# Kernel optimization log

Hardware: AMD Instinct MI355X
Metric: run time of the kernel (lower is better)

Reference implementation:

```python
import jax, jax.numpy as jnp
import numpy as np

K = 9          # kernel_size
PAD = K // 2   # 'same' padding, stride 1
SIGMA = 1.0
EPS = 1e-5     # BatchNorm eps

def _windows(a):
    # a: (B, C, L) -> (B, C, K, L); zero-padded sliding windows (== F.unfold semantics)
    L = a.shape[-1]
    ap = jnp.pad(a, ((0, 0), (0, 0), (PAD, PAD)))
    return jnp.stack([ap[:, :, k:k + L] for k in range(K)], axis=2)

def setup_inputs() -> dict:
    key = jax.random.key(0)
    ks = jax.random.split(key, 4)
    B, Cin, Cout, L = 8, 256, 256, 16384
    x = jax.random.normal(ks[0], (B, Cin, L), jnp.float32)
    coords = jax.random.uniform(ks[1], (B, 3, L), jnp.float32)
    conv_w = jax.random.normal(ks[2], (Cout, Cin, K), jnp.float32) * np.float32(1.0 / np.sqrt(Cin * K))
    conv_b = jnp.zeros((Cout,), jnp.float32)
    gamma = jnp.ones((Cout,), jnp.float32)
    beta = jnp.zeros((Cout,), jnp.float32)
    return {"x": x, "coords": coords, "conv_w": conv_w, "conv_b": conv_b, "gamma": gamma, "beta": beta}

def reference(x, coords, conv_w, conv_b, gamma, beta):
    # --- WeightedConv1D: Gaussian coordinate weights on each unfolded window element ---
    cw = _windows(coords)                                      # (B, 3, K, L)
    d2 = jnp.sum((cw - coords[:, :, None, :]) ** 2, axis=1)    # (B, K, L) squared dist to window center
    w = jnp.exp(-d2 / (2.0 * SIGMA ** 2))                      # (B, K, L) Gaussian weights
    xw = _windows(x) * w[:, None, :, :]                        # (B, Cin, K, L) weighted windows
    y = jnp.einsum('bckl,ock->bol', xw, conv_w) + conv_b[None, :, None]  # (B, Cout, L)
    # --- BatchNorm1d (training-mode batch statistics, biased variance) + ReLU ---
    mu = jnp.mean(y, axis=(0, 2), keepdims=True)
    var = jnp.var(y, axis=(0, 2), keepdims=True)
    yhat = (y - mu) * jax.lax.rsqrt(var + EPS)
    out = jax.nn.relu(yhat * gamma[None, :, None] + beta[None, :, None])
    # Dropout with drop=0.0 is the identity.
    return out
```

## Files before the change

### kernel.cpp

```cpp
#include <hip/hip_runtime.h>
#include <hip/hip_bf16.h>


typedef float        f32x4  __attribute__((ext_vector_type(4)));
typedef float        f32x2  __attribute__((ext_vector_type(2)));
typedef short        bf16x8 __attribute__((ext_vector_type(8)));
typedef unsigned int u32x4  __attribute__((ext_vector_type(4)));

#define LLEN 16384

__device__ __forceinline__ unsigned short bf16bits(float a) {
  return __builtin_bit_cast(unsigned short, __float2bfloat16(a));
}
__device__ __forceinline__ unsigned cvt_pk_bf16(float lo, float hi) {
  unsigned r;
  asm("v_cvt_pk_bf16_f32 %0, %1, %2" : "=v"(r) : "v"(lo), "v"(hi));
  return r;
}

__global__ void k_prep(const float* __restrict__ cw,
                       unsigned short* __restrict__ Aperm,
                       float* __restrict__ sums) {
  const int idx = blockIdx.x * 256 + threadIdx.x;
  if (idx < 512) sums[idx] = 0.0f;
  const int o   = idx / 2304;
  const int rem = idx - o * 2304;
  const int c   = rem / 9;
  const int kk  = rem - c * 9;
  Aperm[((size_t)kk * 256 + o) * 256 + c] = bf16bits(cw[idx]);
}

__global__ void k_w(const float* __restrict__ coords, float* __restrict__ wbuf) {
  const int gidx = blockIdx.x * 256 + threadIdx.x;
  const int b = gidx >> 14, l = gidx & (LLEN - 1);
  const float* cb = coords + (size_t)b * 3 * LLEN;
  const float c0 = cb[l], c1 = cb[LLEN + l], c2v = cb[2 * LLEN + l];
#pragma unroll
  for (int kk = 0; kk < 9; ++kk) {
    const int lc = l + kk - 4;
    float a0 = 0.f, a1 = 0.f, a2 = 0.f;
    if (lc >= 0 && lc < LLEN) { a0 = cb[lc]; a1 = cb[LLEN + lc]; a2 = cb[2 * LLEN + lc]; }
    const float d0 = a0 - c0, d1 = a1 - c1, d2 = a2 - c2v;
    wbuf[(((size_t)(b * 9 + kk)) << 14) + l] = __expf(-0.5f * (d0 * d0 + d1 * d1 + d2 * d2));
  }
}

__global__ __launch_bounds__(512, 2) void k_gemm(
    const float* __restrict__ x, const float* __restrict__ wbuf,
    const unsigned short* __restrict__ Aperm, const float* __restrict__ convb,
    float* __restrict__ y, float* __restrict__ sums) {
  __shared__ __align__(16) unsigned short Ash[2][256 * 64];
  __shared__ __align__(16) unsigned short Xsh[2][264 * 72];

  const int tid  = threadIdx.x;
  const int lane = tid & 63, wv = tid >> 6;
  const int wm = wv >> 2, wn = wv & 3;
  const int hi = lane >> 4, lo16 = lane & 15;
  const int b  = blockIdx.x >> 6, lt = blockIdx.x & 63;
  const int l0 = lt << 8;
  const int nbase = wn * 64 + lo16;
  const int c = tid >> 3, rg = tid & 7;

  f32x4 acc[8][4];
#pragma unroll
  for (int i = 0; i < 8; ++i)
#pragma unroll
    for (int j = 0; j < 4; ++j) acc[i][j] = f32x4{0.f, 0.f, 0.f, 0.f};

  auto loadA = [&](int kk, int cc, u32x4 (&dst)[4]) {
#pragma unroll
    for (int p = 0; p < 4; ++p) {
      const int row = p * 64 + (tid >> 3);
      dst[p] = *reinterpret_cast<const u32x4*>(
          Aperm + ((size_t)kk * 256 + row) * 256 + cc * 64 + ((tid & 7) << 3));
    }
  };
  auto writeA = [&](int ab, const u32x4 (&src)[4]) {
#pragma unroll
    for (int p = 0; p < 4; ++p) {
      const int row  = p * 64 + (tid >> 3);
      const unsigned byte = (unsigned)(row * 128 + (((tid & 7) ^ (row & 7)) << 4));
      *reinterpret_cast<u32x4*>(reinterpret_cast<char*>(&Ash[ab][0]) + byte) = src[p];
    }
  };
  auto loadPiece = [&](int ncc, int i) -> f32x4 {
    const float* xrow = x + ((size_t)(b * 256 + ncc * 64 + c)) * LLEN;
    const int grp = rg + 8 * i;
    const int lx = l0 - 4 + grp * 4;
    f32x4 v = {0.f, 0.f, 0.f, 0.f};
    if (grp < 66 && lx >= 0 && lx <= LLEN - 4)
      v = *reinterpret_cast<const f32x4*>(xrow + lx);
    return v;
  };
  auto writePiece = [&](int xb, int i, const f32x4& v) {
    const int grp = rg + 8 * i;
    if (grp < 66) {
      unsigned short* base = &Xsh[xb][0] + (grp * 4) * 72 + c;
      base[0]   = bf16bits(v[0]);
      base[72]  = bf16bits(v[1]);
      base[144] = bf16bits(v[2]);
      base[216] = bf16bits(v[3]);
    }
  };

  {
    u32x4 a0[4];
    loadA(0, 0, a0);
    writeA(0, a0);
#pragma unroll
    for (int i = 0; i < 9; ++i) writePiece(0, i, loadPiece(0, i));
  }
  float wl[4];
#pragma unroll
  for (int nt = 0; nt < 4; ++nt)
    wl[nt] = wbuf[((size_t)(b * 9) << 14) + l0 + nbase + nt * 16];
  __syncthreads();

  int ab = 0;
  f32x4 xhold = {0.f, 0.f, 0.f, 0.f};

#pragma unroll 1
  for (int cc = 0; cc < 4; ++cc) {
    const int xb = cc & 1;
#pragma unroll 1
    for (int kk = 0; kk < 9; ++kk) {
      const int nkk = (kk == 8) ? 0 : kk + 1;
      const int ncc = (kk == 8) ? cc + 1 : cc;
      const bool has_next = (ncc < 4);

      u32x4 areg[4];
      if (has_next) loadA(nkk, ncc, areg);
      float wln[4] = {0.f, 0.f, 0.f, 0.f};
      if (has_next) {
#pragma unroll
        for (int nt = 0; nt < 4; ++nt)
          wln[nt] = wbuf[((size_t)(b * 9 + nkk) << 14) + l0 + nbase + nt * 16];
      }
      f32x4 xnew = {0.f, 0.f, 0.f, 0.f};
      if (cc < 3) xnew = loadPiece(cc + 1, kk);

      const char* AshB = reinterpret_cast<const char*>(&Ash[ab][0]);
      const char* XshB = reinterpret_cast<const char*>(&Xsh[xb][0]);
#pragma unroll
      for (int kb = 0; kb < 2; ++kb) {
        bf16x8 bfr[4];
#pragma unroll
        for (int nt = 0; nt < 4; ++nt) {
          const int r = nbase + nt * 16 + kk;
          const u32x4 xv = *reinterpret_cast<const u32x4*>(XshB + r * 144 + kb * 64 + hi * 16);
          const float wv2 = wl[nt];
          u32x4 o4;
#pragma unroll
          for (int q = 0; q < 4; ++q) {
            f32x2 f = {__builtin_bit_cast(float, xv[q] << 16),
                       __builtin_bit_cast(float, xv[q] & 0xffff0000u)};
            f *= wv2;
            o4[q] = cvt_pk_bf16(f[0], f[1]);
          }
          bfr[nt] = __builtin_bit_cast(bf16x8, o4);
        }
#pragma unroll
        for (int mt = 0; mt < 8; ++mt) {
          const int orow = wm * 128 + mt * 16 + lo16;
          const unsigned aoff = (unsigned)(orow * 128 + (((kb * 4 + hi) ^ (orow & 7)) << 4));
          const bf16x8 af = *reinterpret_cast<const bf16x8*>(AshB + aoff);
#pragma unroll
          for (int nt = 0; nt < 4; ++nt)
            acc[mt][nt] = __builtin_amdgcn_mfma_f32_16x16x32_bf16(af, bfr[nt],
                                                                  acc[mt][nt], 0, 0, 0);
        }
      }

      if (cc < 3 && kk >= 1) writePiece(xb ^ 1, kk - 1, xhold);
      if (cc < 3 && kk == 8) writePiece(xb ^ 1, 8, xnew);
      if (has_next) writeA(ab ^ 1, areg);

      __syncthreads();
      ab ^= 1;
      xhold = xnew;
#pragma unroll
      for (int nt = 0; nt < 4; ++nt) wl[nt] = wln[nt];
    }
  }

  float* red = reinterpret_cast<float*>(&Ash[0][0]);
  red[tid] = 0.0f;
  __syncthreads();
#pragma unroll
  for (int mt = 0; mt < 8; ++mt) {
#pragma unroll
    for (int v = 0; v < 4; ++v) {
      const int o = wm * 128 + mt * 16 + hi * 4 + v;
      const float cb = convb[o];
      float s = 0.f, s2 = 0.f;
#pragma unroll
      for (int nt = 0; nt < 4; ++nt) {
        const int l = l0 + nbase + nt * 16;
        const float yv = acc[mt][nt][v] + cb;
        y[(((size_t)b * 256 + o) << 14) + l] = yv;
        s += yv; s2 += yv * yv;
      }
#pragma unroll
      for (int d = 1; d < 16; d <<= 1) { s += __shfl_xor(s, d); s2 += __shfl_xor(s2, d); }
      if (lo16 == 0) { atomicAdd(&red[o], s); atomicAdd(&red[o + 256], s2); }
    }
  }
  __syncthreads();
  atomicAdd(&sums[tid], red[tid]);
}

__global__ void k_norm(float* __restrict__ y, const float* __restrict__ sums,
                       const float* __restrict__ gamma, const float* __restrict__ beta) {
  const size_t i0 = ((size_t)blockIdx.x * 256 + threadIdx.x) * 8;
  const int o = (int)((i0 >> 14) & 255);
  const float n = 131072.f;
  const float mu = sums[o] / n;
  float var = sums[256 + o] / n - mu * mu;
  var = fmaxf(var, 0.f);
  const float sc = rsqrtf(var + 1e-5f) * gamma[o];
  const float bb = beta[o] - mu * sc;
  f32x4 v0 = *reinterpret_cast<const f32x4*>(y + i0);
  f32x4 v1 = *reinterpret_cast<const f32x4*>(y + i0 + 4);
#pragma unroll
  for (int i = 0; i < 4; ++i) {
    v0[i] = fmaxf(v0[i] * sc + bb, 0.f);
    v1[i] = fmaxf(v1[i] * sc + bb, 0.f);
  }
  *reinterpret_cast<f32x4*>(y + i0) = v0;
  *reinterpret_cast<f32x4*>(y + i0 + 4) = v1;
}

extern "C" void kernel_launch(void* const* d_in, const int* in_sizes, int n_in,
                              void* d_out, int out_size, void* d_ws, size_t ws_size,
                              hipStream_t stream) {
  const float* x      = (const float*)d_in[0];
  const float* coords = (const float*)d_in[1];
  const float* conv_w = (const float*)d_in[2];
  const float* conv_b = (const float*)d_in[3];
  const float* gamma  = (const float*)d_in[4];
  const float* beta   = (const float*)d_in[5];
  float* out = (float*)d_out;

  float* sums = (float*)d_ws;
  float* wbuf = (float*)((char*)d_ws + 4096);
  unsigned short* Aperm =
      (unsigned short*)((char*)d_ws + 4096 + (size_t)8 * 9 * LLEN * 4);

  k_prep<<<2304, 256, 0, stream>>>(conv_w, Aperm, sums);
  k_w<<<512, 256, 0, stream>>>(coords, wbuf);
  k_gemm<<<512, 512, 0, stream>>>(x, wbuf, Aperm, conv_b, out, sums);
  k_norm<<<16384, 256, 0, stream>>>(out, sums, gamma, beta);
}
```

Baseline: 247.0 us.

## Add pre-transposed bf16 x and direct global-to-LDS DMA GEMM path

Adds a kernel that converts x to bf16 and transposes it into an L-major, swizzled layout, plus a pre-swizzled weight copy, so the GEMM can fill LDS with global_load_lds DMA instead of register-staged loads. The GEMM switches from 16x16x32 to 32x32x16 MFMA tiles and uses a zero buffer for boundary padding. The new path runs only when the workspace is large enough; otherwise the old kernel is used. It adds an extra pass over x (read fp32, write bf16) and more workspace in exchange for cheaper, asynchronous loads inside the GEMM.

```diff
diff --git a/kernel.cpp b/kernel.cpp
--- a/kernel.cpp
+++ b/kernel.cpp
@@ -3,7 +3,7 @@
 
 
 typedef float        f32x4  __attribute__((ext_vector_type(4)));
-typedef float        f32x2  __attribute__((ext_vector_type(2)));
+typedef float        f32x16 __attribute__((ext_vector_type(16)));
 typedef short        bf16x8 __attribute__((ext_vector_type(8)));
 typedef unsigned int u32x4  __attribute__((ext_vector_type(4)));
 
@@ -17,17 +17,29 @@
   asm("v_cvt_pk_bf16_f32 %0, %1, %2" : "=v"(r) : "v"(lo), "v"(hi));
   return r;
 }
+__device__ __forceinline__ void gload16(const void* g, void* l) {
+  __builtin_amdgcn_global_load_lds(
+      (const __attribute__((address_space(1))) unsigned int*)g,
+      (__attribute__((address_space(3))) unsigned int*)l, 16, 0, 0);
+}
 
 __global__ void k_prep(const float* __restrict__ cw,
-                       unsigned short* __restrict__ Aperm,
-                       float* __restrict__ sums) {
+                       unsigned short* __restrict__ A_r4,
+                       unsigned short* __restrict__ A_gl,
+                       float* __restrict__ sums, int big) {
   const int idx = blockIdx.x * 256 + threadIdx.x;
-  if (idx < 512) sums[idx] = 0.0f;
+  if (idx < 1024) sums[idx] = 0.0f;
   const int o   = idx / 2304;
   const int rem = idx - o * 2304;
   const int c   = rem / 9;
   const int kk  = rem - c * 9;
-  Aperm[((size_t)kk * 256 + o) * 256 + c] = bf16bits(cw[idx]);
+  const unsigned short bits = bf16bits(cw[idx]);
+  A_r4[((size_t)kk * 256 + o) * 256 + c] = bits;
+  if (big) {
+    const int cc = c >> 6, c6 = c & 63;
+    const int u = (c6 >> 3) ^ (o & 7);
+    A_gl[(size_t)((kk * 4 + cc) << 14) + ((o * 8 + u) << 3) + (c6 & 7)] = bits;
+  }
 }
 
 __global__ void k_w(const float* __restrict__ coords, float* __restrict__ wbuf) {
@@ -45,7 +57,166 @@
   }
 }
 
-__global__ __launch_bounds__(512, 2) void k_gemm(
+__global__ void k_xT(const float* __restrict__ x, unsigned short* __restrict__ xT) {
+  __shared__ unsigned short T[64][72];
+  const int tid = threadIdx.x, bid = blockIdx.x;
+  const int ct = bid & 3, lt = (bid >> 2) & 255, b = bid >> 10;
+  const int l0 = lt << 6, c0 = ct << 6;
+#pragma unroll
+  for (int p = 0; p < 4; ++p) {
+    const int cl = p * 16 + (tid >> 4), ll = (tid & 15) << 2;
+    const f32x4 v = *reinterpret_cast<const f32x4*>(
+        x + (((size_t)(b * 256 + c0 + cl)) << 14) + l0 + ll);
+#pragma unroll
+    for (int q = 0; q < 4; ++q) T[cl][ll + q] = bf16bits(v[q]);
+  }
+  __syncthreads();
+#pragma unroll
+  for (int pass = 0; pass < 2; ++pass) {
+    const int n = tid + pass * 256;
+    const int ll = n >> 3, u = n & 7;
+    const int l = l0 + ll;
+    const int gsl = (u ^ (l & 7)) << 3;
+    u32x4 val;
+#pragma unroll
+    for (int q = 0; q < 4; ++q)
+      val[q] = (unsigned)T[gsl + 2 * q][ll] | ((unsigned)T[gsl + 2 * q + 1][ll] << 16);
+    *reinterpret_cast<u32x4*>(xT + (((size_t)((b << 14) + l)) << 8) + (ct << 6) + (u << 3)) = val;
+  }
+}
+
+__global__ __launch_bounds__(512, 2) void k_gemm_dma(
+    const unsigned short* __restrict__ xT, const float* __restrict__ wbuf,
+    const unsigned short* __restrict__ Agl, const float* __restrict__ convb,
+    const unsigned short* __restrict__ zeros, float* __restrict__ y,
+    float* __restrict__ sums) {
+  __shared__ __align__(16) unsigned short Ash[2][16384];
+  __shared__ __align__(16) unsigned short Xsh[2][17408];
+
+  const int tid = threadIdx.x, lane = tid & 63, wv = tid >> 6;
+  const int wm = wv >> 2, wn = wv & 3;
+  const int l31 = lane & 31, hi5 = lane >> 5;
+  const int b = blockIdx.x >> 6, lt = blockIdx.x & 63, l0 = lt << 8;
+
+  f32x16 acc[4][2];
+#pragma unroll
+  for (int i = 0; i < 4; ++i)
+#pragma unroll
+    for (int j = 0; j < 2; ++j) acc[i][j] = (f32x16)(0.0f);
+
+  auto dmaA = [&](int ab, int kk, int cc) {
+#pragma unroll
+    for (int call = 0; call < 4; ++call) {
+      const int n0 = ((call << 3) + wv) << 6;
+      gload16(Agl + (((size_t)((kk << 2) + cc)) << 14) + (((size_t)(n0 + lane)) << 3),
+              (char*)&Ash[ab][0] + n0 * 16);
+    }
+  };
+  auto dmaX = [&](int xb, int ncc, int slot) {
+    const int id = (slot << 3) + wv;
+    if (id < 34) {
+      const int n0 = id << 6;
+      const int n = n0 + lane;
+      const int r = n >> 3, u = n & 7;
+      const int lp = l0 - 4 + r;
+      const unsigned short* src =
+          (lp >= 0 && lp < LLEN)
+              ? xT + (((size_t)((b << 14) + lp)) << 8) + (ncc << 6) + (u << 3)
+              : zeros;
+      gload16(src, (char*)&Xsh[xb][0] + n0 * 16);
+    }
+  };
+
+  dmaA(0, 0, 0);
+#pragma unroll
+  for (int s = 0; s < 5; ++s) dmaX(0, 0, s);
+  float wl[2], wt[2];
+#pragma unroll
+  for (int nt = 0; nt < 2; ++nt)
+    wl[nt] = wbuf[((size_t)(b * 9) << 14) + l0 + wn * 64 + nt * 32 + l31];
+  __syncthreads();
+
+  int ab = 0;
+#pragma unroll 1
+  for (int cc = 0; cc < 4; ++cc) {
+    const int xb = cc & 1;
+    const char* XshB = (const char*)&Xsh[xb][0];
+#pragma unroll 1
+    for (int kk = 0; kk < 9; ++kk) {
+      const bool last = (cc == 3) && (kk == 8);
+      const int nkk = (kk == 8) ? 0 : kk + 1;
+      const int ncc = (kk == 8) ? cc + 1 : cc;
+      if (!last) {
+        dmaA(ab ^ 1, nkk, ncc);
+#pragma unroll
+        for (int nt = 0; nt < 2; ++nt)
+          wt[nt] = wbuf[((size_t)(b * 9 + nkk) << 14) + l0 + wn * 64 + nt * 32 + l31];
+      }
+      if (cc < 3 && kk < 5) dmaX(xb ^ 1, cc + 1, kk);
+
+      const char* AshB = (const char*)&Ash[ab][0];
+#pragma unroll
+      for (int ks = 0; ks < 4; ++ks) {
+        const int g = (ks << 1) + hi5;
+        bf16x8 bfr[2];
+#pragma unroll
+        for (int nt = 0; nt < 2; ++nt) {
+          const int rr = wn * 64 + nt * 32 + l31 + kk;
+          const u32x4 xv = *reinterpret_cast<const u32x4*>(
+              XshB + rr * 128 + ((g ^ ((rr + 4) & 7)) << 4));
+          u32x4 o4;
+#pragma unroll
+          for (int q = 0; q < 4; ++q) {
+            const float flo = __builtin_bit_cast(float, xv[q] << 16) * wl[nt];
+            const float fhi = __builtin_bit_cast(float, xv[q] & 0xffff0000u) * wl[nt];
+            o4[q] = cvt_pk_bf16(flo, fhi);
+          }
+          bfr[nt] = __builtin_bit_cast(bf16x8, o4);
+        }
+#pragma unroll
+        for (int mt = 0; mt < 4; ++mt) {
+          const int o = wm * 128 + mt * 32 + l31;
+          const bf16x8 af = *reinterpret_cast<const bf16x8*>(
+              AshB + o * 128 + ((g ^ (l31 & 7)) << 4));
+#pragma unroll
+          for (int nt = 0; nt < 2; ++nt)
+            acc[mt][nt] = __builtin_amdgcn_mfma_f32_32x32x16_bf16(af, bfr[nt],
+                                                                  acc[mt][nt], 0, 0, 0);
+        }
+      }
+      __syncthreads();
+      ab ^= 1;
+      wl[0] = wt[0]; wl[1] = wt[1];
+    }
+  }
+
+  float* red = reinterpret_cast<float*>(&Xsh[0][0]);
+  red[tid] = 0.0f;
+  __syncthreads();
+#pragma unroll
+  for (int mt = 0; mt < 4; ++mt) {
+#pragma unroll
+    for (int v = 0; v < 16; ++v) {
+      const int o = wm * 128 + mt * 32 + (v & 3) + 8 * (v >> 2) + 4 * hi5;
+      const float cb = convb[o];
+      float s = 0.f, s2 = 0.f;
+#pragma unroll
+      for (int nt = 0; nt < 2; ++nt) {
+        const int l = l0 + wn * 64 + nt * 32 + l31;
+        const float yv = acc[mt][nt][v] + cb;
+        y[(((size_t)b * 256 + o) << 14) + l] = yv;
+        s += yv; s2 += yv * yv;
+      }
+#pragma unroll
+      for (int d = 1; d < 32; d <<= 1) { s += __shfl_xor(s, d); s2 += __shfl_xor(s2, d); }
+      if (l31 == 0) { atomicAdd(&red[o], s); atomicAdd(&red[o + 256], s2); }
+    }
+  }
+  __syncthreads();
+  atomicAdd(&sums[tid], red[tid]);
+}
+
+__global__ __launch_bounds__(512, 2) void k_gemm_fb(
     const float* __restrict__ x, const float* __restrict__ wbuf,
     const unsigned short* __restrict__ Aperm, const float* __restrict__ convb,
     float* __restrict__ y, float* __restrict__ sums) {
@@ -152,10 +323,9 @@
           u32x4 o4;
 #pragma unroll
           for (int q = 0; q < 4; ++q) {
-            f32x2 f = {__builtin_bit_cast(float, xv[q] << 16),
-                       __builtin_bit_cast(float, xv[q] & 0xffff0000u)};
-            f *= wv2;
-            o4[q] = cvt_pk_bf16(f[0], f[1]);
+            const float flo = __builtin_bit_cast(float, xv[q] << 16) * wv2;
+            const float fhi = __builtin_bit_cast(float, xv[q] & 0xffff0000u) * wv2;
+            o4[q] = cvt_pk_bf16(flo, fhi);
           }
           bfr[nt] = __builtin_bit_cast(bf16x8, o4);
         }
@@ -242,12 +412,21 @@
   float* out = (float*)d_out;
 
   float* sums = (float*)d_ws;
+  const unsigned short* zeros = (const unsigned short*)((char*)d_ws + 2048);
   float* wbuf = (float*)((char*)d_ws + 4096);
-  unsigned short* Aperm =
-      (unsigned short*)((char*)d_ws + 4096 + (size_t)8 * 9 * LLEN * 4);
-
-  k_prep<<<2304, 256, 0, stream>>>(conv_w, Aperm, sums);
+  unsigned short* A_r4 = (unsigned short*)((char*)d_ws + 4096 + (size_t)8 * 9 * LLEN * 4);
+  unsigned short* A_gl = A_r4 + 589824;
+  unsigned short* xT   = A_gl + 589824;
+  const size_t need = 4096 + (size_t)8 * 9 * LLEN * 4 + 2 * 1179648ull + 67108864ull;
+  const int big = (ws_size >= need) ? 1 : 0;
+
+  k_prep<<<2304, 256, 0, stream>>>(conv_w, A_r4, A_gl, sums, big);
   k_w<<<512, 256, 0, stream>>>(coords, wbuf);
-  k_gemm<<<512, 512, 0, stream>>>(x, wbuf, Aperm, conv_b, out, sums);
+  if (big) {
+    k_xT<<<8192, 256, 0, stream>>>(x, xT);
+    k_gemm_dma<<<512, 512, 0, stream>>>(xT, wbuf, A_gl, conv_b, zeros, out, sums);
+  } else {
+    k_gemm_fb<<<512, 512, 0, stream>>>(x, wbuf, A_r4, conv_b, out, sums);
+  }
   k_norm<<<16384, 256, 0, stream>>>(out, sums, gamma, beta);
 }
```

Result: slower. 287.5 us (+16.4%).
